# Performance work log

Measured on AMD Instinct MI355X. Metric: run time of the kernel, lower is better.

The kernel has to match this reference:

```python
import jax, jax.numpy as jnp
import numpy as np

N = 8192
IN_F = 512
OUT_F = 256

def setup_inputs() -> dict:
    key = jax.random.key(0)
    k1, k2, k3 = jax.random.split(key, 3)
    A = jax.random.uniform(k1, (N, N), dtype=jnp.float32)
    X = jax.random.normal(k2, (N, IN_F), dtype=jnp.float32)
    init_range = np.sqrt(6.0 / (IN_F + OUT_F)).astype(np.float32)
    W = jax.random.uniform(k3, (IN_F, OUT_F), dtype=jnp.float32,
                           minval=-init_range, maxval=init_range)
    return {"weighted_adjacency_matrix": A, "feature_matrix": X, "weight": W}

def reference(weighted_adjacency_matrix, feature_matrix, weight):
    A = weighted_adjacency_matrix
    # d = (1 + row_sum(A))^{-1/2}; D^{-1/2} A D^{-1/2} via row/col broadcast scaling
    d = jax.lax.rsqrt(1.0 + jnp.sum(A, axis=1))            # [N]
    norm_adj = d[:, None] * A * d[None, :]                  # [N, N]
    support = feature_matrix @ weight                       # [N, out_features]
    return norm_adj @ support                               # [N, out_features]
```

## Files before the change

kernel.cpp:

```cpp
#include <hip/hip_runtime.h>
#include <hip/hip_bf16.h>
#include <stdint.h>

#define NROW 8192
#define INF  512
#define OUTF 256

typedef __attribute__((ext_vector_type(8))) short bf16x8;
typedef __attribute__((ext_vector_type(4))) float f32x4;

__device__ __forceinline__ unsigned short f2bf(float x) {
  union { float f; unsigned u; } v; v.f = x;
  unsigned r = v.u + 0x7fffu + ((v.u >> 16) & 1u);
  return (unsigned short)(r >> 16);
}

__device__ __forceinline__ void async_cp16(const void* g, void* l) {
  __builtin_amdgcn_global_load_lds((const __attribute__((address_space(1))) void*)g,
                                   (__attribute__((address_space(3))) void*)l,
                                   16, 0, 0);
}

__global__ __launch_bounds__(256) void k_rowsum_convert(
    const float* __restrict__ A, unsigned short* __restrict__ Ab,
    float* __restrict__ dv) {
  int w = threadIdx.x >> 6, lane = threadIdx.x & 63;
  int row = blockIdx.x * 4 + w;
  const float4* ar = (const float4*)(A + (size_t)row * NROW);
  ushort4* br = (ushort4*)(Ab + (size_t)row * NROW);
  float s = 0.f;
  #pragma unroll 4
  for (int it = 0; it < NROW / 256; ++it) {
    float4 v = ar[it * 64 + lane];
    s += (v.x + v.y) + (v.z + v.w);
    ushort4 b; b.x = f2bf(v.x); b.y = f2bf(v.y); b.z = f2bf(v.z); b.w = f2bf(v.w);
    br[it * 64 + lane] = b;
  }
  #pragma unroll
  for (int off = 32; off > 0; off >>= 1) s += __shfl_down(s, off, 64);
  if (lane == 0) dv[row] = rsqrtf(1.f + s);
}

__global__ __launch_bounds__(256) void k_convert_x(
    const float4* __restrict__ X4, ushort4* __restrict__ Xs4) {
  int q = blockIdx.x * 256 + threadIdx.x;
  float4 v = X4[q];
  ushort4 h; h.x = f2bf(v.x); h.y = f2bf(v.y); h.z = f2bf(v.z); h.w = f2bf(v.w);
  Xs4[q] = h;
}

__global__ __launch_bounds__(256) void k_convert_w(
    const float* __restrict__ W, unsigned short* __restrict__ WsT) {
  int idx = blockIdx.x * 256 + threadIdx.x;
  int k = idx >> 8, f = idx & 255;
  WsT[(size_t)f * INF + k] = f2bf(W[idx]);
}

template<int KTOT, int KSPLIT, bool EPI>
__global__ __launch_bounds__(256, 2) void k_gemm_bt(
    const unsigned short* __restrict__ Aop,
    const unsigned short* __restrict__ Bop,
    float* __restrict__ Pout,
    unsigned short* __restrict__ Yout,
    const float* __restrict__ dv) {
  constexpr int KPS = KTOT / KSPLIT;
  constexpr int NITER = KPS / 64;
  __shared__ unsigned short lA[128 * 64];
  __shared__ unsigned short lB[128 * 64];
  const int t = threadIdx.x;
  const int w = t >> 6, lane = t & 63;
  const int m0 = blockIdx.x * 128;
  const int n0 = blockIdx.y * 128;
  const int kz = blockIdx.z * KPS;
  const int rsub = lane >> 3;
  const int csub = lane & 7;
  const int swz = csub ^ rsub;
  const int lr = lane & 15, lq = lane >> 4, x7 = lane & 7;
  const int mw = (w >> 1) * 64, nw = (w & 1) * 64;

  f32x4 zero = {0.f, 0.f, 0.f, 0.f};
  f32x4 acc[4][4];
  #pragma unroll
  for (int i = 0; i < 4; ++i) {
    #pragma unroll
    for (int j = 0; j < 4; ++j) acc[i][j] = zero;
  }

  const unsigned short* ga0 = Aop + (size_t)(m0 + w * 8 + rsub) * KTOT + kz + swz * 8;
  const unsigned short* gb0 = Bop + (size_t)(n0 + w * 8 + rsub) * KTOT + kz + swz * 8;

  for (int it = 0; it < NITER; ++it) {
    __syncthreads();
    #pragma unroll
    for (int i = 0; i < 4; ++i) {
      async_cp16(ga0 + (size_t)(i * 32) * KTOT + it * 64, &lA[(i * 32 + w * 8) * 64]);
      async_cp16(gb0 + (size_t)(i * 32) * KTOT + it * 64, &lB[(i * 32 + w * 8) * 64]);
    }
    __syncthreads();
    #pragma unroll
    for (int ks = 0; ks < 2; ++ks) {
      bf16x8 af[4], bfv[4];
      #pragma unroll
      for (int mi = 0; mi < 4; ++mi) {
        int r = mw + mi * 16 + lr;
        af[mi] = *(const bf16x8*)&lA[r * 64 + (((ks * 4 + lq) ^ x7) << 3)];
      }
      #pragma unroll
      for (int ni = 0; ni < 4; ++ni) {
        int r = nw + ni * 16 + lr;
        bfv[ni] = *(const bf16x8*)&lB[r * 64 + (((ks * 4 + lq) ^ x7) << 3)];
      }
      #pragma unroll
      for (int mi = 0; mi < 4; ++mi) {
        #pragma unroll
        for (int ni = 0; ni < 4; ++ni) {
          acc[mi][ni] = __builtin_amdgcn_mfma_f32_16x16x32_bf16(
              af[mi], bfv[ni], acc[mi][ni], 0, 0, 0);
        }
      }
    }
  }

  #pragma unroll
  for (int mi = 0; mi < 4; ++mi) {
    #pragma unroll
    for (int ni = 0; ni < 4; ++ni) {
      f32x4 a = acc[mi][ni];
      int gr0 = m0 + mw + mi * 16 + lq * 4;
      int gc  = n0 + nw + ni * 16 + lr;
      if constexpr (EPI) {
        #pragma unroll
        for (int r = 0; r < 4; ++r) {
          int gr = gr0 + r;
          Yout[(size_t)gr * OUTF + gc] = f2bf(dv[gr] * a[r]);
        }
      } else {
        float* P = Pout + (size_t)blockIdx.z * NROW * OUTF;
        #pragma unroll
        for (int r = 0; r < 4; ++r) {
          P[(size_t)(gr0 + r) * OUTF + gc] = a[r];
        }
      }
    }
  }
}

__global__ __launch_bounds__(256) void k_transpose(
    const unsigned short* __restrict__ Y, unsigned short* __restrict__ YT) {
  __shared__ unsigned short T[64][72];
  int i0 = blockIdx.x * 64, f0 = blockIdx.y * 64;
  int t = threadIdx.x;
  int rr = t >> 4, cc = t & 15;
  #pragma unroll
  for (int p = 0; p < 4; ++p) {
    int r = p * 16 + rr;
    ushort4 v = *(const ushort4*)&Y[(size_t)(i0 + r) * OUTF + f0 + cc * 4];
    T[cc * 4 + 0][r] = v.x; T[cc * 4 + 1][r] = v.y;
    T[cc * 4 + 2][r] = v.z; T[cc * 4 + 3][r] = v.w;
  }
  __syncthreads();
  #pragma unroll
  for (int p = 0; p < 4; ++p) {
    int fr = p * 16 + rr;
    ushort4 v;
    v.x = T[fr][cc * 4 + 0]; v.y = T[fr][cc * 4 + 1];
    v.z = T[fr][cc * 4 + 2]; v.w = T[fr][cc * 4 + 3];
    *(ushort4*)&YT[(size_t)(f0 + fr) * NROW + i0 + cc * 4] = v;
  }
}

__global__ __launch_bounds__(256) void k_reduce(
    const float4* __restrict__ P4, const float* __restrict__ dv,
    float4* __restrict__ o4) {
  int q = blockIdx.x * 256 + threadIdx.x;
  const int QT = NROW * OUTF / 4;
  float4 a = P4[q], b = P4[QT + q], c = P4[2 * QT + q], e = P4[3 * QT + q];
  float dd = dv[q >> 6];
  float4 r;
  r.x = dd * ((a.x + b.x) + (c.x + e.x));
  r.y = dd * ((a.y + b.y) + (c.y + e.y));
  r.z = dd * ((a.z + b.z) + (c.z + e.z));
  r.w = dd * ((a.w + b.w) + (c.w + e.w));
  o4[q] = r;
}

__global__ __launch_bounds__(256) void k_rowsum_only(
    const float* __restrict__ A, float* __restrict__ dv) {
  int w = threadIdx.x >> 6, lane = threadIdx.x & 63;
  int row = blockIdx.x * 4 + w;
  const float4* ar = (const float4*)(A + (size_t)row * NROW);
  float s = 0.f;
  for (int it = 0; it < NROW / 256; ++it) {
    float4 v = ar[it * 64 + lane];
    s += (v.x + v.y) + (v.z + v.w);
  }
  #pragma unroll
  for (int off = 32; off > 0; off >>= 1) s += __shfl_down(s, off, 64);
  if (lane == 0) dv[row] = rsqrtf(1.f + s);
}

__global__ __launch_bounds__(256) void k_support_naive(
    const float* __restrict__ X, const float* __restrict__ W,
    const float* __restrict__ dv, float* __restrict__ Y) {
  __shared__ float lX[INF];
  int i = blockIdx.x;
  for (int k = threadIdx.x; k < INF; k += 256) lX[k] = X[(size_t)i * INF + k];
  __syncthreads();
  int f = threadIdx.x;
  float s = 0.f;
  for (int k = 0; k < INF; ++k) s += lX[k] * W[(size_t)k * OUTF + f];
  Y[(size_t)i * OUTF + f] = dv[i] * s;
}

__global__ __launch_bounds__(256) void k_main_naive(
    const float* __restrict__ A, const float* __restrict__ Y,
    const float* __restrict__ dv, float* __restrict__ out) {
  __shared__ float lA[256];
  int i = blockIdx.x, f = threadIdx.x;
  float s = 0.f;
  for (int jb = 0; jb < NROW; jb += 256) {
    __syncthreads();
    lA[threadIdx.x] = A[(size_t)i * NROW + jb + threadIdx.x];
    __syncthreads();
    for (int jj = 0; jj < 256; ++jj) s += lA[jj] * Y[(size_t)(jb + jj) * OUTF + f];
  }
  out[(size_t)i * OUTF + f] = dv[i] * s;
}

extern "C" void kernel_launch(void* const* d_in, const int* in_sizes, int n_in,
                              void* d_out, int out_size, void* d_ws, size_t ws_size,
                              hipStream_t stream) {
  const float* A = (const float*)d_in[0];
  const float* X = (const float*)d_in[1];
  const float* W = (const float*)d_in[2];
  float* out = (float*)d_out;

  const size_t SZ_AB  = (size_t)NROW * NROW * 2;
  const size_t SZ_YT  = (size_t)OUTF * NROW * 2;
  const size_t SZ_XS  = (size_t)NROW * INF * 2;
  const size_t SZ_WST = (size_t)OUTF * INF * 2;
  const size_t SZ_YB  = (size_t)NROW * OUTF * 2;
  const size_t SZ_D   = (size_t)NROW * 4;
  const size_t SZ_P   = (size_t)4 * NROW * OUTF * 4;
  const size_t NEED = SZ_AB + SZ_YT + SZ_XS + SZ_WST + SZ_YB + SZ_D + SZ_P;

  char* p = (char*)d_ws;
  if (ws_size >= NEED) {
    unsigned short* Ab  = (unsigned short*)p; p += SZ_AB;
    unsigned short* YT  = (unsigned short*)p; p += SZ_YT;
    unsigned short* Xs  = (unsigned short*)p; p += SZ_XS;
    unsigned short* WsT = (unsigned short*)p; p += SZ_WST;
    unsigned short* Yb  = (unsigned short*)p; p += SZ_YB;
    float* dv = (float*)p; p += SZ_D;
    float* P  = (float*)p;

    k_rowsum_convert<<<dim3(2048), dim3(256), 0, stream>>>(A, Ab, dv);
    k_convert_x<<<dim3(4096), dim3(256), 0, stream>>>((const float4*)X, (ushort4*)Xs);
    k_convert_w<<<dim3(512), dim3(256), 0, stream>>>(W, WsT);
    k_gemm_bt<INF, 1, true><<<dim3(64, 2, 1), dim3(256), 0, stream>>>(
        Xs, WsT, nullptr, Yb, dv);
    k_transpose<<<dim3(128, 4), dim3(256), 0, stream>>>(Yb, YT);
    k_gemm_bt<NROW, 4, false><<<dim3(64, 2, 4), dim3(256), 0, stream>>>(
        Ab, YT, P, nullptr, nullptr);
    k_reduce<<<dim3(2048), dim3(256), 0, stream>>>((const float4*)P, dv, (float4*)out);
  } else {
    float* dv = (float*)p; p += SZ_D;
    float* Y  = (float*)p;
    k_rowsum_only<<<dim3(2048), dim3(256), 0, stream>>>(A, dv);
    k_support_naive<<<dim3(8192), dim3(256), 0, stream>>>(X, W, dv, Y);
    k_main_naive<<<dim3(8192), dim3(256), 0, stream>>>(A, Y, dv, out);
  }
}
```

Measured before the change: 473.0 us.

## Widen main GEMM tile to full 256 columns, write support pre-transposed, split-K by 8

The main GEMM now gives each block 128 rows by all 256 output columns with an 8-way K split. Each block of A is read from global memory once instead of twice, and the grid still has 512 blocks. The support GEMM computes W^T·X^T so it writes the d-scaled result directly in transposed layout, which removes the separate transpose kernel and its buffer. A bf16 conversion with simpler rounding is used for A. The costs are a larger partial-sum buffer and reduction pass (8 slices), higher register pressure from the 4x8 accumulator tiles, and uncoalesced strided stores in the support epilogue.

```diff
diff --git a/kernel.cpp b/kernel.cpp
--- a/kernel.cpp
+++ b/kernel.cpp
@@ -13,6 +13,10 @@
   union { float f; unsigned u; } v; v.f = x;
   unsigned r = v.u + 0x7fffu + ((v.u >> 16) & 1u);
   return (unsigned short)(r >> 16);
+}
+__device__ __forceinline__ unsigned short f2bf_fast(float x) {
+  union { float f; unsigned u; } v; v.f = x;
+  return (unsigned short)((v.u + 0x8000u) >> 16);
 }
 
 __device__ __forceinline__ void async_cp16(const void* g, void* l) {
@@ -33,7 +37,9 @@
   for (int it = 0; it < NROW / 256; ++it) {
     float4 v = ar[it * 64 + lane];
     s += (v.x + v.y) + (v.z + v.w);
-    ushort4 b; b.x = f2bf(v.x); b.y = f2bf(v.y); b.z = f2bf(v.z); b.w = f2bf(v.w);
+    ushort4 b;
+    b.x = f2bf_fast(v.x); b.y = f2bf_fast(v.y);
+    b.z = f2bf_fast(v.z); b.w = f2bf_fast(v.w);
     br[it * 64 + lane] = b;
   }
   #pragma unroll
@@ -56,71 +62,55 @@
   WsT[(size_t)f * INF + k] = f2bf(W[idx]);
 }
 
-template<int KTOT, int KSPLIT, bool EPI>
-__global__ __launch_bounds__(256, 2) void k_gemm_bt(
-    const unsigned short* __restrict__ Aop,
-    const unsigned short* __restrict__ Bop,
-    float* __restrict__ Pout,
-    unsigned short* __restrict__ Yout,
-    const float* __restrict__ dv) {
-  constexpr int KPS = KTOT / KSPLIT;
-  constexpr int NITER = KPS / 64;
+__global__ __launch_bounds__(256, 2) void k_support(
+    const unsigned short* __restrict__ WsT,
+    const unsigned short* __restrict__ Xs,
+    const float* __restrict__ dv,
+    unsigned short* __restrict__ YT) {
   __shared__ unsigned short lA[128 * 64];
   __shared__ unsigned short lB[128 * 64];
   const int t = threadIdx.x;
   const int w = t >> 6, lane = t & 63;
   const int m0 = blockIdx.x * 128;
   const int n0 = blockIdx.y * 128;
-  const int kz = blockIdx.z * KPS;
-  const int rsub = lane >> 3;
-  const int csub = lane & 7;
-  const int swz = csub ^ rsub;
+  const int rsub = lane >> 3, csub = lane & 7, swz = csub ^ rsub;
   const int lr = lane & 15, lq = lane >> 4, x7 = lane & 7;
   const int mw = (w >> 1) * 64, nw = (w & 1) * 64;
 
-  f32x4 zero = {0.f, 0.f, 0.f, 0.f};
   f32x4 acc[4][4];
   #pragma unroll
-  for (int i = 0; i < 4; ++i) {
-    #pragma unroll
-    for (int j = 0; j < 4; ++j) acc[i][j] = zero;
-  }
-
-  const unsigned short* ga0 = Aop + (size_t)(m0 + w * 8 + rsub) * KTOT + kz + swz * 8;
-  const unsigned short* gb0 = Bop + (size_t)(n0 + w * 8 + rsub) * KTOT + kz + swz * 8;
-
-  for (int it = 0; it < NITER; ++it) {
+  for (int i = 0; i < 4; ++i)
+    #pragma unroll
+    for (int j = 0; j < 4; ++j) acc[i][j] = f32x4{0.f, 0.f, 0.f, 0.f};
+
+  const unsigned short* ga0 = WsT + (size_t)(m0 + w * 8 + rsub) * INF + swz * 8;
+  const unsigned short* gb0 = Xs  + (size_t)(n0 + w * 8 + rsub) * INF + swz * 8;
+
+  for (int it = 0; it < INF / 64; ++it) {
     __syncthreads();
     #pragma unroll
     for (int i = 0; i < 4; ++i) {
-      async_cp16(ga0 + (size_t)(i * 32) * KTOT + it * 64, &lA[(i * 32 + w * 8) * 64]);
-      async_cp16(gb0 + (size_t)(i * 32) * KTOT + it * 64, &lB[(i * 32 + w * 8) * 64]);
+      async_cp16(ga0 + (size_t)(i * 32) * INF + it * 64, &lA[(i * 32 + w * 8) * 64]);
+      async_cp16(gb0 + (size_t)(i * 32) * INF + it * 64, &lB[(i * 32 + w * 8) * 64]);
     }
     __syncthreads();
     #pragma unroll
     for (int ks = 0; ks < 2; ++ks) {
       bf16x8 af[4], bfv[4];
       #pragma unroll
-      for (int mi = 0; mi < 4; ++mi) {
-        int r = mw + mi * 16 + lr;
-        af[mi] = *(const bf16x8*)&lA[r * 64 + (((ks * 4 + lq) ^ x7) << 3)];
-      }
-      #pragma unroll
-      for (int ni = 0; ni < 4; ++ni) {
-        int r = nw + ni * 16 + lr;
-        bfv[ni] = *(const bf16x8*)&lB[r * 64 + (((ks * 4 + lq) ^ x7) << 3)];
-      }
-      #pragma unroll
-      for (int mi = 0; mi < 4; ++mi) {
+      for (int mi = 0; mi < 4; ++mi)
+        af[mi] = *(const bf16x8*)&lA[(mw + mi * 16 + lr) * 64 + (((ks * 4 + lq) ^ x7) << 3)];
+      #pragma unroll
+      for (int ni = 0; ni < 4; ++ni)
+        bfv[ni] = *(const bf16x8*)&lB[(nw + ni * 16 + lr) * 64 + (((ks * 4 + lq) ^ x7) << 3)];
+      #pragma unroll
+      for (int mi = 0; mi < 4; ++mi)
         #pragma unroll
-        for (int ni = 0; ni < 4; ++ni) {
+        for (int ni = 0; ni < 4; ++ni)
           acc[mi][ni] = __builtin_amdgcn_mfma_f32_16x16x32_bf16(
               af[mi], bfv[ni], acc[mi][ni], 0, 0, 0);
-        }
-      }
-    }
-  }
-
+    }
+  }
   #pragma unroll
   for (int mi = 0; mi < 4; ++mi) {
     #pragma unroll
@@ -128,60 +118,94 @@
       f32x4 a = acc[mi][ni];
       int gr0 = m0 + mw + mi * 16 + lq * 4;
       int gc  = n0 + nw + ni * 16 + lr;
-      if constexpr (EPI) {
+      float dd = dv[gc];
+      #pragma unroll
+      for (int r = 0; r < 4; ++r)
+        YT[(size_t)(gr0 + r) * NROW + gc] = f2bf(dd * a[r]);
+    }
+  }
+}
+
+__global__ __launch_bounds__(256, 2) void k_gemm_main(
+    const unsigned short* __restrict__ Ab,
+    const unsigned short* __restrict__ YT,
+    float* __restrict__ P) {
+  __shared__ unsigned short lA[128 * 64];
+  __shared__ unsigned short lB[256 * 64];
+  const int t = threadIdx.x;
+  const int w = t >> 6, lane = t & 63;
+  const int m0 = blockIdx.x * 128;
+  const int kz = blockIdx.y * 1024;
+  const int rsub = lane >> 3, csub = lane & 7, swz = csub ^ rsub;
+  const int lr = lane & 15, lq = lane >> 4, x7 = lane & 7;
+  const int mw = (w & 1) * 64;
+  const int nw = (w >> 1) * 128;
+
+  f32x4 acc[4][8];
+  #pragma unroll
+  for (int i = 0; i < 4; ++i)
+    #pragma unroll
+    for (int j = 0; j < 8; ++j) acc[i][j] = f32x4{0.f, 0.f, 0.f, 0.f};
+
+  const unsigned short* ga0 = Ab + (size_t)(m0 + w * 8 + rsub) * NROW + kz + swz * 8;
+  const unsigned short* gb0 = YT + (size_t)(w * 8 + rsub) * NROW + kz + swz * 8;
+
+  for (int it = 0; it < 16; ++it) {
+    __syncthreads();
+    #pragma unroll
+    for (int i = 0; i < 4; ++i)
+      async_cp16(ga0 + (size_t)(i * 32) * NROW + it * 64, &lA[(i * 32 + w * 8) * 64]);
+    #pragma unroll
+    for (int i = 0; i < 8; ++i)
+      async_cp16(gb0 + (size_t)(i * 32) * NROW + it * 64, &lB[(i * 32 + w * 8) * 64]);
+    __syncthreads();
+    #pragma unroll
+    for (int ks = 0; ks < 2; ++ks) {
+      bf16x8 af[4], bfv[8];
+      #pragma unroll
+      for (int mi = 0; mi < 4; ++mi)
+        af[mi] = *(const bf16x8*)&lA[(mw + mi * 16 + lr) * 64 + (((ks * 4 + lq) ^ x7) << 3)];
+      #pragma unroll
+      for (int ni = 0; ni < 8; ++ni)
+        bfv[ni] = *(const bf16x8*)&lB[(nw + ni * 16 + lr) * 64 + (((ks * 4 + lq) ^ x7) << 3)];
+      #pragma unroll
+      for (int mi = 0; mi < 4; ++mi)
         #pragma unroll
-        for (int r = 0; r < 4; ++r) {
-          int gr = gr0 + r;
-          Yout[(size_t)gr * OUTF + gc] = f2bf(dv[gr] * a[r]);
-        }
-      } else {
-        float* P = Pout + (size_t)blockIdx.z * NROW * OUTF;
-        #pragma unroll
-        for (int r = 0; r < 4; ++r) {
-          P[(size_t)(gr0 + r) * OUTF + gc] = a[r];
-        }
-      }
-    }
-  }
-}
-
-__global__ __launch_bounds__(256) void k_transpose(
-    const unsigned short* __restrict__ Y, unsigned short* __restrict__ YT) {
-  __shared__ unsigned short T[64][72];
-  int i0 = blockIdx.x * 64, f0 = blockIdx.y * 64;
-  int t = threadIdx.x;
-  int rr = t >> 4, cc = t & 15;
-  #pragma unroll
-  for (int p = 0; p < 4; ++p) {
-    int r = p * 16 + rr;
-    ushort4 v = *(const ushort4*)&Y[(size_t)(i0 + r) * OUTF + f0 + cc * 4];
-    T[cc * 4 + 0][r] = v.x; T[cc * 4 + 1][r] = v.y;
-    T[cc * 4 + 2][r] = v.z; T[cc * 4 + 3][r] = v.w;
-  }
-  __syncthreads();
-  #pragma unroll
-  for (int p = 0; p < 4; ++p) {
-    int fr = p * 16 + rr;
-    ushort4 v;
-    v.x = T[fr][cc * 4 + 0]; v.y = T[fr][cc * 4 + 1];
-    v.z = T[fr][cc * 4 + 2]; v.w = T[fr][cc * 4 + 3];
-    *(ushort4*)&YT[(size_t)(f0 + fr) * NROW + i0 + cc * 4] = v;
-  }
-}
-
-__global__ __launch_bounds__(256) void k_reduce(
+        for (int ni = 0; ni < 8; ++ni)
+          acc[mi][ni] = __builtin_amdgcn_mfma_f32_16x16x32_bf16(
+              af[mi], bfv[ni], acc[mi][ni], 0, 0, 0);
+    }
+  }
+
+  float* Pz = P + (size_t)blockIdx.y * NROW * OUTF;
+  #pragma unroll
+  for (int mi = 0; mi < 4; ++mi) {
+    #pragma unroll
+    for (int ni = 0; ni < 8; ++ni) {
+      f32x4 a = acc[mi][ni];
+      int gr0 = m0 + mw + mi * 16 + lq * 4;
+      int gc  = nw + ni * 16 + lr;
+      #pragma unroll
+      for (int r = 0; r < 4; ++r)
+        Pz[(size_t)(gr0 + r) * OUTF + gc] = a[r];
+    }
+  }
+}
+
+__global__ __launch_bounds__(256) void k_reduce8(
     const float4* __restrict__ P4, const float* __restrict__ dv,
     float4* __restrict__ o4) {
   int q = blockIdx.x * 256 + threadIdx.x;
   const int QT = NROW * OUTF / 4;
-  float4 a = P4[q], b = P4[QT + q], c = P4[2 * QT + q], e = P4[3 * QT + q];
+  float4 s = P4[q];
+  #pragma unroll
+  for (int z = 1; z < 8; ++z) {
+    float4 v = P4[(size_t)z * QT + q];
+    s.x += v.x; s.y += v.y; s.z += v.z; s.w += v.w;
+  }
   float dd = dv[q >> 6];
-  float4 r;
-  r.x = dd * ((a.x + b.x) + (c.x + e.x));
-  r.y = dd * ((a.y + b.y) + (c.y + e.y));
-  r.z = dd * ((a.z + b.z) + (c.z + e.z));
-  r.w = dd * ((a.w + b.w) + (c.w + e.w));
-  o4[q] = r;
+  s.x *= dd; s.y *= dd; s.z *= dd; s.w *= dd;
+  o4[q] = s;
 }
 
 __global__ __launch_bounds__(256) void k_rowsum_only(
@@ -239,10 +263,9 @@
   const size_t SZ_YT  = (size_t)OUTF * NROW * 2;
   const size_t SZ_XS  = (size_t)NROW * INF * 2;
   const size_t SZ_WST = (size_t)OUTF * INF * 2;
-  const size_t SZ_YB  = (size_t)NROW * OUTF * 2;
   const size_t SZ_D   = (size_t)NROW * 4;
-  const size_t SZ_P   = (size_t)4 * NROW * OUTF * 4;
-  const size_t NEED = SZ_AB + SZ_YT + SZ_XS + SZ_WST + SZ_YB + SZ_D + SZ_P;
+  const size_t SZ_P   = (size_t)8 * NROW * OUTF * 4;
+  const size_t NEED = SZ_AB + SZ_YT + SZ_XS + SZ_WST + SZ_D + SZ_P;
 
   char* p = (char*)d_ws;
   if (ws_size >= NEED) {
@@ -250,19 +273,15 @@
     unsigned short* YT  = (unsigned short*)p; p += SZ_YT;
     unsigned short* Xs  = (unsigned short*)p; p += SZ_XS;
     unsigned short* WsT = (unsigned short*)p; p += SZ_WST;
-    unsigned short* Yb  = (unsigned short*)p; p += SZ_YB;
     float* dv = (float*)p; p += SZ_D;
     float* P  = (float*)p;
 
     k_rowsum_convert<<<dim3(2048), dim3(256), 0, stream>>>(A, Ab, dv);
     k_convert_x<<<dim3(4096), dim3(256), 0, stream>>>((const float4*)X, (ushort4*)Xs);
     k_convert_w<<<dim3(512), dim3(256), 0, stream>>>(W, WsT);
-    k_gemm_bt<INF, 1, true><<<dim3(64, 2, 1), dim3(256), 0, stream>>>(
-        Xs, WsT, nullptr, Yb, dv);
-    k_transpose<<<dim3(128, 4), dim3(256), 0, stream>>>(Yb, YT);
-    k_gemm_bt<NROW, 4, false><<<dim3(64, 2, 4), dim3(256), 0, stream>>>(
-        Ab, YT, P, nullptr, nullptr);
-    k_reduce<<<dim3(2048), dim3(256), 0, stream>>>((const float4*)P, dv, (float4*)out);
+    k_support<<<dim3(2, 64), dim3(256), 0, stream>>>(WsT, Xs, dv, YT);
+    k_gemm_main<<<dim3(64, 8), dim3(256), 0, stream>>>(Ab, YT, P);
+    k_reduce8<<<dim3(2048), dim3(256), 0, stream>>>((const float4*)P, dv, (float4*)out);
   } else {
     float* dv = (float*)p; p += SZ_D;
     float* Y  = (float*)p;
```

Measured after the change: 460.6 us. -2.6%, faster.
